# Kernel optimization log

Measured on AMD Instinct MI355X. Metric: run time of the kernel, lower is better.

Reference implementation:

```python
import jax, jax.numpy as jnp
import numpy as np

LN2 = 0.6931471805599453

def ssp(x):
    # 'shifted_sp' activation: softplus(x) - log(2)
    return jax.nn.softplus(x) - LN2

def _res_chain(x, W1, b1, W2, b2):
    # PhysNetResidual chain: x <- lin2(ssp(lin1(ssp(x)))) + x
    # W1/W2: [n_res, F, F], b1/b2: [n_res, F]
    for j in range(W1.shape[0]):
        h = ssp(x) @ W1[j] + b1[j]
        x = ssp(h) @ W2[j] + b2[j] + x
    return x

def _physnet_module(feat, radial_aev, idx12, p):
    (W_I, b_I, W_J, b_J, W_gate, gvec, W_int, b_int,
     ri_W1, ri_b1, ri_W2, ri_b2,
     ra_W1, ra_b1, ra_W2, ra_b2,
     ro_W1, ro_b1, ro_W2, ro_b2, W_out, b_out) = p
    N, F = feat.shape
    # self term (no species are dummy -> non_dummy indexing is identity)
    h_self = ssp(ssp(feat) @ W_I + b_I)                       # [N,F]
    # pair messages
    gate = radial_aev @ W_gate                                 # [P,F] (no bias)
    f12 = feat[idx12]                                          # [2,P,F] gather
    fm = ssp(ssp(f12) @ W_J + b_J)                             # [2,P,F]
    pair_msg = gate[None] * fm                                 # [2,P,F]
    proto = jnp.zeros_like(feat).at[idx12.reshape(-1)].add(
        pair_msg.reshape(-1, F))                               # scatter-add
    proto = proto + h_self
    msg = _res_chain(proto, ri_W1, ri_b1, ri_W2, ri_b2)
    feat2 = feat * gvec + ssp(msg) @ W_int + b_int
    feat2 = _res_chain(feat2, ra_W1, ra_b1, ra_W2, ra_b2)
    e = ssp(_res_chain(feat2, ro_W1, ro_b1, ro_W2, ro_b2)) @ W_out + b_out  # [N]
    return e, feat2

def setup_inputs() -> dict:
    key = jax.random.key(0)
    L, F, R = 5, 128, 64
    M, A = 128, 64
    N = M * A
    P = 400000
    ks = jax.random.split(key, 20)
    s = 0.05  # small weight scale keeps activations stable across 5 modules
    inp = {
        'species': jax.random.randint(ks[0], (M, A), 0, 4, dtype=jnp.int32),
        'features': jax.random.normal(ks[1], (N, F), jnp.float32),
        'radial_aev': jax.random.uniform(ks[2], (P, R), jnp.float32),
        'atom_index12': jax.random.randint(ks[3], (2, P), 0, N, dtype=jnp.int32),
        'W_I': jax.random.normal(ks[4], (L, F, F)) * s,
        'b_I': jnp.zeros((L, F)),
        'W_J': jax.random.normal(ks[5], (L, F, F)) * s,
        'b_J': jnp.zeros((L, F)),
        'W_gate': jax.random.normal(ks[6], (L, R, F)) * s,
        'gvec': jnp.ones((L, F)),
        'W_int': jax.random.normal(ks[7], (L, F, F)) * s,
        'b_int': jnp.zeros((L, F)),
        'ri_W1': jax.random.normal(ks[8], (L, 3, F, F)) * s,
        'ri_b1': jnp.zeros((L, 3, F)),
        'ri_W2': jax.random.normal(ks[9], (L, 3, F, F)) * s,
        'ri_b2': jnp.zeros((L, 3, F)),
        'ra_W1': jax.random.normal(ks[10], (L, 2, F, F)) * s,
        'ra_b1': jnp.zeros((L, 2, F)),
        'ra_W2': jax.random.normal(ks[11], (L, 2, F, F)) * s,
        'ra_b2': jnp.zeros((L, 2, F)),
        'ro_W1': jax.random.normal(ks[12], (L, 1, F, F)) * s,
        'ro_b1': jnp.zeros((L, 1, F)),
        'ro_W2': jax.random.normal(ks[13], (L, 1, F, F)) * s,
        'ro_b2': jnp.zeros((L, 1, F)),
        'W_out': jax.random.normal(ks[14], (L, F)) * s,
        'b_out': jnp.zeros((L,)),
    }
    return inp

def reference(species, features, radial_aev, atom_index12,
              W_I, b_I, W_J, b_J, W_gate, gvec, W_int, b_int,
              ri_W1, ri_b1, ri_W2, ri_b2,
              ra_W1, ra_b1, ra_W2, ra_b2,
              ro_W1, ro_b1, ro_W2, ro_b2, W_out, b_out):
    M, A = species.shape
    params = (W_I, b_I, W_J, b_J, W_gate, gvec, W_int, b_int,
              ri_W1, ri_b1, ri_W2, ri_b2,
              ra_W1, ra_b1, ra_W2, ra_b2,
              ro_W1, ro_b1, ro_W2, ro_b2, W_out, b_out)
    feat = features
    energies = jnp.zeros((M * A,), features.dtype)
    for l in range(W_I.shape[0]):  # fixed small module loop
        p = tuple(arr[l] for arr in params)
        e, feat = _physnet_module(feat, radial_aev, atom_index12, p)
        energies = energies + e
    return energies.reshape(M, A), feat
```

## Files before the change

### kernel.cpp

```cpp
#include <hip/hip_runtime.h>


#define LN2F 0.69314718055994530942f
#define NB 128

using short8  = __attribute__((ext_vector_type(8))) short;
using float4v = __attribute__((ext_vector_type(4))) float;
typedef const __attribute__((address_space(1))) unsigned int* gas1_t;
typedef __attribute__((address_space(3))) unsigned int* las3_t;

__device__ __forceinline__ float sspf(float x) {
  float ax = fabsf(x);
  return fmaxf(x, 0.0f) + __logf(1.0f + __expf(-ax)) - LN2F;
}

__device__ __forceinline__ unsigned short f2bf(float x) {
  return (unsigned short)((__float_as_uint(x) + 0x8000u) >> 16);
}

__device__ __forceinline__ unsigned short f2bf_ne(float x) {
  unsigned int u = __float_as_uint(x);
  u += 0x7fffu + ((u >> 16) & 1u);
  return (unsigned short)(u >> 16);
}

__device__ __forceinline__ void dma16(const void* g, void* l) {
  __builtin_amdgcn_global_load_lds((gas1_t)(unsigned long long)g,
                                   (las3_t)(unsigned long long)l, 16, 0, 0);
}

__device__ __forceinline__ void dma32k(const unsigned short* g, unsigned short* l,
                                       int w, int lane) {
  const char* gb = (const char*)g + w * 2048 + lane * 16;
  char* lb = (char*)l + w * 2048;
  dma16(gb, lb);
  dma16(gb + 1024, lb + 1024);
}
__device__ __forceinline__ void dma16k(const unsigned short* g, unsigned short* l,
                                       int w, int lane) {
  dma16((const char*)g + w * 1024 + lane * 16, (char*)l + w * 1024);
}

struct K1Args {
  const float* wsrc[80];
  int isgate[80];
  const float* bp[17];
  int bstride[17];
  const float* b_out;
  const int* idx;
  unsigned short* Wt;
  float* bias_pack;
  unsigned int* H;
  int n2p, C;
};

__global__ __launch_bounds__(256) void k1_prep(K1Args K) {
  __shared__ unsigned int h[8192];
  int b = blockIdx.x, tid = threadIdx.x;
  if (b < 80) {
    const float* s = K.wsrc[b];
    unsigned short* d = K.Wt + (size_t)b * 16384;
    if (!K.isgate[b]) {
      for (int it = 0; it < 8; ++it) {
        int q = tid + it * 256;
        int n = q & 127, j = q >> 7;
        unsigned short tmp[8];
#pragma unroll
        for (int cc = 0; cc < 8; ++cc) tmp[cc] = f2bf_ne(s[(8 * j + cc) * 128 + n]);
        *(uint4*)(d + (n * 16 + (j ^ (n & 15))) * 8) = *(uint4*)tmp;
      }
    } else {
      for (int it = 0; it < 4; ++it) {
        int q = tid + it * 256;
        int n = q & 127, j = q >> 7;
        unsigned short tmp[8];
#pragma unroll
        for (int cc = 0; cc < 8; ++cc) tmp[cc] = f2bf_ne(s[(8 * j + cc) * 128 + n]);
        *(uint4*)(d + (n * 8 + (j ^ (n & 7))) * 8) = *(uint4*)tmp;
      }
    }
  } else if (b < 85) {
    int l = b - 80;
    for (int i = tid; i < 17 * 128; i += 256) {
      int s = i >> 7;
      K.bias_pack[(size_t)l * 2304 + i] = K.bp[s][l * K.bstride[s] + (i & 127)];
    }
    if (tid == 0) K.bias_pack[(size_t)l * 2304 + 17 * 128] = K.b_out[l];
  } else {
    int blk = b - 85;
    for (int i = tid; i < 8192; i += 256) h[i] = 0;
    __syncthreads();
    int s = blk * K.C, e = min(s + K.C, K.n2p);
    for (int i = s + tid; i < e; i += 256) atomicAdd(&h[K.idx[i]], 1u);
    __syncthreads();
    for (int i = tid; i < 8192; i += 256) K.H[(size_t)blk * 8192 + i] = h[i];
  }
}

__global__ __launch_bounds__(256) void col_scan(unsigned int* __restrict__ H,
                                                unsigned int* __restrict__ tot) {
  int a = blockIdx.x * 256 + threadIdx.x;
  unsigned int run = 0;
  for (int b = 0; b < NB; ++b) {
    unsigned int v = H[(size_t)b * 8192 + a];
    H[(size_t)b * 8192 + a] = run;
    run += v;
  }
  tot[a] = run;
}

__global__ __launch_bounds__(256) void place_pass(const int* __restrict__ idx,
                                                  const unsigned int* __restrict__ H,
                                                  const unsigned int* __restrict__ tot,
                                                  unsigned int* __restrict__ off_out,
                                                  unsigned int* __restrict__ pairid,
                                                  int P, int C) {
  __shared__ unsigned int pos[8192];
  __shared__ unsigned int wt4[4];
  int b = blockIdx.x, tid = threadIdx.x;
  unsigned int local[32], s = 0;
#pragma unroll
  for (int i = 0; i < 32; ++i) { local[i] = tot[tid * 32 + i]; s += local[i]; }
  unsigned int v = s;
  int lane = tid & 63, wv = tid >> 6;
#pragma unroll
  for (int o = 1; o < 64; o <<= 1) {
    unsigned int u = __shfl_up(v, o, 64);
    if (lane >= o) v += u;
  }
  if (lane == 63) wt4[wv] = v;
  __syncthreads();
  unsigned int base = 0;
  for (int k = 0; k < wv; ++k) base += wt4[k];
  unsigned int excl = base + v - s;
#pragma unroll
  for (int i = 0; i < 32; ++i) {
    pos[tid * 32 + i] = excl;
    if (b == 0) off_out[tid * 32 + i] = excl;
    excl += local[i];
  }
  if (b == 0 && tid == 255) off_out[8192] = excl;
  __syncthreads();
  for (int i = tid; i < 8192; i += 256) pos[i] += H[(size_t)b * 8192 + i];
  __syncthreads();
  int n2p = 2 * P;
  int s2 = b * C, e2 = min(s2 + C, n2p);
  for (int i = s2 + tid; i < e2; i += 256) {
    int a = idx[i];
    unsigned int p = atomicAdd(&pos[a], 1u);
    pairid[p] = (i >= P) ? (unsigned int)(i - P) : (unsigned int)i;
  }
}

__global__ __launch_bounds__(256) void gather_kernel(const float* __restrict__ radial,
                                                     const unsigned int* __restrict__ off,
                                                     const unsigned int* __restrict__ pairid,
                                                     float* __restrict__ S) {
  __shared__ float4v red[3][16];
  int a = blockIdx.x;
  int lane = threadIdx.x & 63, w = threadIdx.x >> 6;
  int grp = lane >> 4, l16v = lane & 15;
  unsigned int b = off[a], e = off[a + 1];
  float4v acc = {0.f, 0.f, 0.f, 0.f};
  for (unsigned int base = b; base < e; base += 128) {
    unsigned int pp[8];
#pragma unroll
    for (int k = 0; k < 8; ++k) {
      unsigned int j = base + k * 16 + w * 4 + grp;
      pp[k] = pairid[j < e ? j : b];
    }
    float4v vv[8];
#pragma unroll
    for (int k = 0; k < 8; ++k)
      vv[k] = *(const float4v*)(radial + (size_t)pp[k] * 64 + l16v * 4);
#pragma unroll
    for (int k = 0; k < 8; ++k) {
      unsigned int j = base + k * 16 + w * 4 + grp;
      if (j < e) acc += vv[k];
    }
  }
#pragma unroll
  for (int o = 16; o < 64; o <<= 1) {
#pragma unroll
    for (int cc = 0; cc < 4; ++cc) acc[cc] += __shfl_xor(acc[cc], o, 64);
  }
  if (w > 0 && grp == 0) red[w - 1][l16v] = acc;
  __syncthreads();
  if (w == 0 && grp == 0) {
    acc += red[0][l16v];
    acc += red[1][l16v];
    acc += red[2][l16v];
    *(float4v*)(S + (size_t)a * 64 + l16v * 4) = acc;
  }
}

struct ChainArgs {
  const float* feat_in;
  const float* S;
  const unsigned short* wt;
  const float* bias_pack;
  float* feat_out;
  float* energy;
};

#define MFMA_ __builtin_amdgcn_mfma_f32_16x16x32_bf16

#define G128(AP, SP, ACC) { \
  short8 a0_ = *(const short8*)(aB + (AP)*4352); \
  short8 a1_ = *(const short8*)(aB + (AP)*4352 + 32); \
  short8 a2_ = *(const short8*)(aB + (AP)*4352 + 64); \
  short8 a3_ = *(const short8*)(aB + (AP)*4352 + 96); \
  ACC = MFMA_(a0_, *(const short8*)(b0 + (SP)*16384), ACC, 0, 0, 0); \
  ACC = MFMA_(a1_, *(const short8*)(b1 + (SP)*16384), ACC, 0, 0, 0); \
  ACC = MFMA_(a2_, *(const short8*)(b2 + (SP)*16384), ACC, 0, 0, 0); \
  ACC = MFMA_(a3_, *(const short8*)(b3 + (SP)*16384), ACC, 0, 0, 0); }

#define WSSPM(AP, V) { \
  wB[(AP)*4352]       = f2bf(sspf((V)[0])); \
  wB[(AP)*4352 + 136] = f2bf(sspf((V)[1])); \
  wB[(AP)*4352 + 272] = f2bf(sspf((V)[2])); \
  wB[(AP)*4352 + 408] = f2bf(sspf((V)[3])); }

#define MODBODY(S0) { \
  const float* bl = &sB[(S0)][0]; \
   \
  dma32k(wtp + 2*16384, swb[(S0)^1], w, lane); \
  gG = Z; \
  { short8 s0_ = *(const short8*)(aS); short8 s1_ = *(const short8*)(aS + 32); \
    gG = MFMA_(s0_, *(const short8*)(g0), gG, 0, 0, 0); \
    gG = MFMA_(s1_, *(const short8*)(g1), gG, 0, 0, 0); } \
  fm = Z; G128(0, (S0), fm); \
  { float bv = bl[col0]; \
    for (int r = 0; r < 4; ++r) fm[r] = sspf(fm[r] + bv); } \
  __syncthreads(); \
   \
  dma32k(wtp + 3*16384, swb[(S0)], w, lane); \
  if (l < 4) dma16k(wtp + 16*16384, sG, w, lane); \
  t4 = Z; G128(0, (S0)^1, t4); \
  { float bv = bl[128 + col0]; \
    for (int r = 0; r < 4; ++r) xf[r] = fm[r]*gG[r] + sspf(t4[r] + bv); } \
  WSSPM(1, xf); \
  __syncthreads(); \
   \
  dma32k(wtp + 4*16384, swb[(S0)^1], w, lane); \
  t4 = Z; G128(1, (S0), t4); \
  { float bv = bl[2*128 + col0]; for (int r = 0; r < 4; ++r) t4[r] += bv; } \
  WSSPM(0, t4); __syncthreads(); \
  dma32k(wtp + 5*16384, swb[(S0)], w, lane); \
  t4 = Z; G128(0, (S0)^1, t4); \
  { float bv = bl[3*128 + col0]; for (int r = 0; r < 4; ++r) xf[r] += t4[r] + bv; } \
  WSSPM(1, xf); __syncthreads(); \
  dma32k(wtp + 6*16384, swb[(S0)^1], w, lane); \
  t4 = Z; G128(1, (S0), t4); \
  { float bv = bl[4*128 + col0]; for (int r = 0; r < 4; ++r) t4[r] += bv; } \
  WSSPM(0, t4); __syncthreads(); \
  dma32k(wtp + 7*16384, swb[(S0)], w, lane); \
  t4 = Z; G128(0, (S0)^1, t4); \
  { float bv = bl[5*128 + col0]; for (int r = 0; r < 4; ++r) xf[r] += t4[r] + bv; } \
  WSSPM(1, xf); __syncthreads(); \
  dma32k(wtp + 8*16384, swb[(S0)^1], w, lane); \
  t4 = Z; G128(1, (S0), t4); \
  { float bv = bl[6*128 + col0]; for (int r = 0; r < 4; ++r) t4[r] += bv; } \
  WSSPM(0, t4); __syncthreads(); \
  dma32k(wtp + 9*16384, swb[(S0)], w, lane); \
  t4 = Z; G128(0, (S0)^1, t4); \
  { float bv = bl[7*128 + col0]; for (int r = 0; r < 4; ++r) xf[r] += t4[r] + bv; } \
  WSSPM(1, xf); __syncthreads(); \
   \
  dma32k(wtp + 10*16384, swb[(S0)^1], w, lane); \
  t4 = Z; G128(1, (S0), t4); \
  { float bv = bl[8*128 + col0]; float gv = bl[15*128 + col0]; \
    for (int r = 0; r < 4; ++r) xf[r] = ff[r]*gv + t4[r] + bv; } \
  WSSPM(0, xf); __syncthreads(); \
   \
  dma32k(wtp + 11*16384, swb[(S0)], w, lane); \
  t4 = Z; G128(0, (S0)^1, t4); \
  { float bv = bl[9*128 + col0]; for (int r = 0; r < 4; ++r) t4[r] += bv; } \
  WSSPM(1, t4); __syncthreads(); \
  dma32k(wtp + 12*16384, swb[(S0)^1], w, lane); \
  t4 = Z; G128(1, (S0), t4); \
  { float bv = bl[10*128 + col0]; for (int r = 0; r < 4; ++r) xf[r] += t4[r] + bv; } \
  WSSPM(0, xf); __syncthreads(); \
  dma32k(wtp + 13*16384, swb[(S0)], w, lane); \
  t4 = Z; G128(0, (S0)^1, t4); \
  { float bv = bl[11*128 + col0]; for (int r = 0; r < 4; ++r) t4[r] += bv; } \
  WSSPM(1, t4); __syncthreads(); \
  dma32k(wtp + 14*16384, swb[(S0)^1], w, lane); \
  if (l < 4 && w < 9) \
    dma16((const char*)A.bias_pack + (size_t)(l + 1) * 9216 + w * 1024 + lane * 16, \
          (char*)&sB[(S0)^1][0] + w * 1024); \
  t4 = Z; G128(1, (S0), t4); \
  { float bv = bl[12*128 + col0]; for (int r = 0; r < 4; ++r) xf[r] += t4[r] + bv; } \
  WSSPM(0, xf); __syncthreads(); \
  ff = xf; \
  if (l == 4) { \
    for (int r = 0; r < 4; ++r) \
      A.feat_out[(size_t)(row0 + arow + quad*4 + r) * 128 + col0] = xf[r]; \
  } \
   \
  dma32k(wtp + 15*16384, swb[(S0)], w, lane); \
  t4 = Z; G128(0, (S0)^1, t4); \
  { float bv = bl[13*128 + col0]; for (int r = 0; r < 4; ++r) t4[r] += bv; } \
  WSSPM(1, t4); __syncthreads(); \
   \
  if (l < 4) dma32k(wtp + 17*16384, swb[(S0)^1], w, lane); \
  t4 = Z; G128(1, (S0), t4); \
  { float bv = bl[14*128 + col0]; float wv = bl[16*128 + col0]; \
    p0 += sspf(xf[0] + t4[0] + bv) * wv; \
    p1 += sspf(xf[1] + t4[1] + bv) * wv; \
    p2 += sspf(xf[2] + t4[2] + bv) * wv; \
    p3 += sspf(xf[3] + t4[3] + bv) * wv; } \
  bsum += bl[17*128]; \
  __syncthreads(); }

__global__ __launch_bounds__(1024, 4) void chain_kernel(ChainArgs A) {
  __shared__ __align__(16) unsigned short swb[2][16384];
  __shared__ __align__(16) unsigned short sG[8192];
  __shared__ __align__(16) unsigned short sA[2][32 * 136];
  __shared__ __align__(16) unsigned short sS[32 * 72];
  __shared__ __align__(16) float sB[2][2304];
  __shared__ float sE[32];

  const int tid  = threadIdx.x;
  const int row0 = blockIdx.x * 32;
  const int lane = tid & 63;
  const int w    = tid >> 6;
  const int g    = w >> 3;
  const int c    = w & 7;
  const int l16  = lane & 15;
  const int quad = lane >> 4;
  const int arow = 16 * g;
  const int col0 = 16 * c + l16;
  const int l8   = l16 & 7;

  const unsigned short* aB = &sA[0][0] + (arow + l16) * 136 + quad * 8;
  unsigned short*       wB = &sA[0][0] + (arow + quad * 4) * 136 + col0;
  const unsigned short* b0 = &swb[0][0] + col0 * 128 + (((quad + 0) ^ l16) * 8);
  const unsigned short* b1 = &swb[0][0] + col0 * 128 + (((quad + 4) ^ l16) * 8);
  const unsigned short* b2 = &swb[0][0] + col0 * 128 + (((quad + 8) ^ l16) * 8);
  const unsigned short* b3 = &swb[0][0] + col0 * 128 + (((quad + 12) ^ l16) * 8);
  const unsigned short* aS = &sS[0] + (arow + l16) * 72 + quad * 8;
  const unsigned short* g0 = &sG[0] + col0 * 64 + (((quad + 0) ^ l8) * 8);
  const unsigned short* g1 = &sG[0] + col0 * 64 + (((quad + 4) ^ l8) * 8);

  dma16k(A.wt, sG, w, lane);
  dma32k(A.wt + 16384, swb[0], w, lane);
  if (w < 9)
    dma16((const char*)A.bias_pack + w * 1024 + lane * 16, (char*)&sB[0][0] + w * 1024);

  for (int i = tid; i < 32 * 64; i += 1024) {
    int r = i >> 6, k = i & 63;
    sS[r * 72 + k] = f2bf(A.S[(size_t)(row0 + r) * 64 + k]);
  }
  for (int i = tid; i < 32 * 128; i += 1024) {
    int r = i >> 7, k = i & 127;
    sA[0][r * 136 + k] = f2bf(sspf(A.feat_in[(size_t)(row0 + r) * 128 + k]));
  }
  float4v ff;
#pragma unroll
  for (int r = 0; r < 4; ++r)
    ff[r] = A.feat_in[(size_t)(row0 + arow + quad * 4 + r) * 128 + col0];
  if (tid < 32) sE[tid] = 0.0f;
  __syncthreads();

  const float4v Z = {0.f, 0.f, 0.f, 0.f};
  float4v gG, fm, xf, t4;
  float p0 = 0.f, p1 = 0.f, p2 = 0.f, p3 = 0.f, bsum = 0.f;

#pragma unroll 1
  for (int l = 0; l < 5; ++l) {
    const unsigned short* wtp = A.wt + (size_t)l * 16 * 16384;
    if ((l & 1) == 0) MODBODY(0) else MODBODY(1)
  }

#pragma unroll
  for (int o = 1; o < 16; o <<= 1) {
    p0 += __shfl_xor(p0, o, 64);
    p1 += __shfl_xor(p1, o, 64);
    p2 += __shfl_xor(p2, o, 64);
    p3 += __shfl_xor(p3, o, 64);
  }
  if (l16 == 0) {
    atomicAdd(&sE[arow + quad * 4 + 0], p0);
    atomicAdd(&sE[arow + quad * 4 + 1], p1);
    atomicAdd(&sE[arow + quad * 4 + 2], p2);
    atomicAdd(&sE[arow + quad * 4 + 3], p3);
  }
  __syncthreads();
  if (tid < 32) A.energy[row0 + tid] = sE[tid] + bsum;
}

extern "C" void kernel_launch(void* const* d_in, const int* in_sizes, int n_in,
                              void* d_out, int out_size, void* d_ws, size_t ws_size,
                              hipStream_t stream) {
  const float* features = (const float*)d_in[1];
  const float* radial   = (const float*)d_in[2];
  const int*   idx12    = (const int*)  d_in[3];
  const float* W_I    = (const float*)d_in[4];
  const float* b_I    = (const float*)d_in[5];
  const float* W_J    = (const float*)d_in[6];
  const float* b_J    = (const float*)d_in[7];
  const float* W_gate = (const float*)d_in[8];
  const float* gvec   = (const float*)d_in[9];
  const float* W_int  = (const float*)d_in[10];
  const float* b_int  = (const float*)d_in[11];
  const float* ri_W1  = (const float*)d_in[12];
  const float* ri_b1  = (const float*)d_in[13];
  const float* ri_W2  = (const float*)d_in[14];
  const float* ri_b2  = (const float*)d_in[15];
  const float* ra_W1  = (const float*)d_in[16];
  const float* ra_b1  = (const float*)d_in[17];
  const float* ra_W2  = (const float*)d_in[18];
  const float* ra_b2  = (const float*)d_in[19];
  const float* ro_W1  = (const float*)d_in[20];
  const float* ro_b1  = (const float*)d_in[21];
  const float* ro_W2  = (const float*)d_in[22];
  const float* ro_b2  = (const float*)d_in[23];
  const float* W_out  = (const float*)d_in[24];
  const float* b_out  = (const float*)d_in[25];

  const int N = in_sizes[1] / 128;
  const int P = in_sizes[3] / 2;
  const int L = in_sizes[25];
  const int n2p = 2 * P;
  const int C = (n2p + NB - 1) / NB;

  float* S = (float*)d_ws;
  float* bias_pack = S + (size_t)N * 64;
  unsigned short* Wt = (unsigned short*)(bias_pack + 5 * 2304);
  unsigned int* H      = (unsigned int*)(Wt + (size_t)80 * 16384);
  unsigned int* tot    = H + (size_t)NB * 8192;
  unsigned int* off    = tot + N;
  unsigned int* pairid = off + N + 4;

  K1Args k1;
  for (int l = 0; l < L; ++l) {
    const float* fx[16] = {
      W_gate + l * 8192,
      W_J + l * 16384, W_I + l * 16384,
      ri_W1 + (l * 3 + 0) * 16384, ri_W2 + (l * 3 + 0) * 16384,
      ri_W1 + (l * 3 + 1) * 16384, ri_W2 + (l * 3 + 1) * 16384,
      ri_W1 + (l * 3 + 2) * 16384, ri_W2 + (l * 3 + 2) * 16384,
      W_int + l * 16384,
      ra_W1 + (l * 2 + 0) * 16384, ra_W2 + (l * 2 + 0) * 16384,
      ra_W1 + (l * 2 + 1) * 16384, ra_W2 + (l * 2 + 1) * 16384,
      ro_W1 + l * 16384, ro_W2 + l * 16384 };
    for (int t = 0; t < 16; ++t) { k1.wsrc[l * 16 + t] = fx[t]; k1.isgate[l * 16 + t] = (t == 0); }
  }
  const float* bp[17] = { b_J, b_I,
    ri_b1, ri_b2, ri_b1 + 128, ri_b2 + 128, ri_b1 + 256, ri_b2 + 256,
    b_int, ra_b1, ra_b2, ra_b1 + 128, ra_b2 + 128, ro_b1, ro_b2, gvec, W_out };
  int st[17] = {128,128, 384,384,384,384,384,384, 128, 256,256,256,256, 128,128,128,128};
  for (int q = 0; q < 17; ++q) { k1.bp[q] = bp[q]; k1.bstride[q] = st[q]; }
  k1.b_out = b_out;
  k1.idx = idx12; k1.Wt = Wt; k1.bias_pack = bias_pack; k1.H = H;
  k1.n2p = n2p; k1.C = C;
  k1_prep<<<80 + 5 + NB, 256, 0, stream>>>(k1);

  col_scan<<<32, 256, 0, stream>>>(H, tot);
  place_pass<<<NB, 256, 0, stream>>>(idx12, H, tot, off, pairid, P, C);
  gather_kernel<<<N, 256, 0, stream>>>(radial, off, pairid, S);

  ChainArgs ca;
  ca.feat_in   = features;
  ca.S         = S;
  ca.wt        = Wt;
  ca.bias_pack = bias_pack;
  ca.energy    = (float*)d_out;
  ca.feat_out  = (float*)d_out + N;
  chain_kernel<<<N / 32, 1024, 0, stream>>>(ca);
}
```

Baseline: 328.8 us.

## Fuse preprocessing kernels into one cooperative kernel with grid syncs

Merges weight conversion, bias packing, histogram, column scan, placement and radial gather into a single cooperative kernel of 256 blocks of 1024 threads, separated by grid-wide syncs. It also parallelises the column scan across 32 row segments per column instead of one thread walking all 128 rows. The aim is to remove launch gaps and the serial scan. The trade-off is that grid.sync barriers are added, and the gather now runs on only 256 blocks rather than one block per atom, which may reduce memory-level parallelism.

```diff
diff --git a/kernel.cpp b/kernel.cpp
--- a/kernel.cpp
+++ b/kernel.cpp
@@ -1,4 +1,7 @@
 #include <hip/hip_runtime.h>
+#include <hip/hip_cooperative_groups.h>
+
+namespace cg = cooperative_groups;
 
 
 #define LN2F 0.69314718055994530942f
@@ -41,28 +44,44 @@
   dma16((const char*)g + w * 1024 + lane * 16, (char*)l + w * 1024);
 }
 
-struct K1Args {
+struct SArgs {
   const float* wsrc[80];
   int isgate[80];
   const float* bp[17];
   int bstride[17];
   const float* b_out;
   const int* idx;
+  const float* radial;
   unsigned short* Wt;
   float* bias_pack;
   unsigned int* H;
-  int n2p, C;
+  unsigned int* tot;
+  unsigned int* off;
+  unsigned int* pairid;
+  float* S;
+  int P, n2p, C;
 };
 
-__global__ __launch_bounds__(256) void k1_prep(K1Args K) {
-  __shared__ unsigned int h[8192];
-  int b = blockIdx.x, tid = threadIdx.x;
-  if (b < 80) {
-    const float* s = K.wsrc[b];
-    unsigned short* d = K.Wt + (size_t)b * 16384;
-    if (!K.isgate[b]) {
-      for (int it = 0; it < 8; ++it) {
-        int q = tid + it * 256;
+__global__ __launch_bounds__(1024) void s_all(SArgs K) {
+  __shared__ unsigned int shst[8192];
+  __shared__ unsigned int wtt[16];
+  cg::grid_group grid = cg::this_grid();
+  const int b = blockIdx.x, tid = threadIdx.x;
+
+  if (b < NB) {
+    for (int i = tid; i < 8192; i += 1024) shst[i] = 0;
+    __syncthreads();
+    int s = b * K.C, e = min(s + K.C, K.n2p);
+    for (int i = s + tid; i < e; i += 1024) atomicAdd(&shst[K.idx[i]], 1u);
+    __syncthreads();
+    for (int i = tid; i < 8192; i += 1024) K.H[(size_t)b * 8192 + i] = shst[i];
+  } else if (b < NB + 80) {
+    int m = b - NB;
+    const float* s = K.wsrc[m];
+    unsigned short* d = K.Wt + (size_t)m * 16384;
+    if (!K.isgate[m]) {
+      for (int it = 0; it < 2; ++it) {
+        int q = tid + it * 1024;
         int n = q & 127, j = q >> 7;
         unsigned short tmp[8];
 #pragma unroll
@@ -70,127 +89,123 @@
         *(uint4*)(d + (n * 16 + (j ^ (n & 15))) * 8) = *(uint4*)tmp;
       }
     } else {
-      for (int it = 0; it < 4; ++it) {
-        int q = tid + it * 256;
-        int n = q & 127, j = q >> 7;
-        unsigned short tmp[8];
-#pragma unroll
-        for (int cc = 0; cc < 8; ++cc) tmp[cc] = f2bf_ne(s[(8 * j + cc) * 128 + n]);
-        *(uint4*)(d + (n * 8 + (j ^ (n & 7))) * 8) = *(uint4*)tmp;
-      }
-    }
-  } else if (b < 85) {
-    int l = b - 80;
-    for (int i = tid; i < 17 * 128; i += 256) {
+      int n = tid & 127, j = tid >> 7;
+      unsigned short tmp[8];
+#pragma unroll
+      for (int cc = 0; cc < 8; ++cc) tmp[cc] = f2bf_ne(s[(8 * j + cc) * 128 + n]);
+      *(uint4*)(d + (n * 8 + (j ^ (n & 7))) * 8) = *(uint4*)tmp;
+    }
+  } else if (b < NB + 85) {
+    int l = b - (NB + 80);
+    for (int i = tid; i < 17 * 128; i += 1024) {
       int s = i >> 7;
       K.bias_pack[(size_t)l * 2304 + i] = K.bp[s][l * K.bstride[s] + (i & 127)];
     }
     if (tid == 0) K.bias_pack[(size_t)l * 2304 + 17 * 128] = K.b_out[l];
-  } else {
-    int blk = b - 85;
-    for (int i = tid; i < 8192; i += 256) h[i] = 0;
-    __syncthreads();
-    int s = blk * K.C, e = min(s + K.C, K.n2p);
-    for (int i = s + tid; i < e; i += 256) atomicAdd(&h[K.idx[i]], 1u);
-    __syncthreads();
-    for (int i = tid; i < 8192; i += 256) K.H[(size_t)blk * 8192 + i] = h[i];
-  }
-}
-
-__global__ __launch_bounds__(256) void col_scan(unsigned int* __restrict__ H,
-                                                unsigned int* __restrict__ tot) {
-  int a = blockIdx.x * 256 + threadIdx.x;
-  unsigned int run = 0;
-  for (int b = 0; b < NB; ++b) {
-    unsigned int v = H[(size_t)b * 8192 + a];
-    H[(size_t)b * 8192 + a] = run;
-    run += v;
-  }
-  tot[a] = run;
-}
-
-__global__ __launch_bounds__(256) void place_pass(const int* __restrict__ idx,
-                                                  const unsigned int* __restrict__ H,
-                                                  const unsigned int* __restrict__ tot,
-                                                  unsigned int* __restrict__ off_out,
-                                                  unsigned int* __restrict__ pairid,
-                                                  int P, int C) {
-  __shared__ unsigned int pos[8192];
-  __shared__ unsigned int wt4[4];
-  int b = blockIdx.x, tid = threadIdx.x;
-  unsigned int local[32], s = 0;
-#pragma unroll
-  for (int i = 0; i < 32; ++i) { local[i] = tot[tid * 32 + i]; s += local[i]; }
-  unsigned int v = s;
-  int lane = tid & 63, wv = tid >> 6;
-#pragma unroll
-  for (int o = 1; o < 64; o <<= 1) {
-    unsigned int u = __shfl_up(v, o, 64);
-    if (lane >= o) v += u;
-  }
-  if (lane == 63) wt4[wv] = v;
-  __syncthreads();
-  unsigned int base = 0;
-  for (int k = 0; k < wv; ++k) base += wt4[k];
-  unsigned int excl = base + v - s;
-#pragma unroll
-  for (int i = 0; i < 32; ++i) {
-    pos[tid * 32 + i] = excl;
-    if (b == 0) off_out[tid * 32 + i] = excl;
-    excl += local[i];
-  }
-  if (b == 0 && tid == 255) off_out[8192] = excl;
-  __syncthreads();
-  for (int i = tid; i < 8192; i += 256) pos[i] += H[(size_t)b * 8192 + i];
-  __syncthreads();
-  int n2p = 2 * P;
-  int s2 = b * C, e2 = min(s2 + C, n2p);
-  for (int i = s2 + tid; i < e2; i += 256) {
-    int a = idx[i];
-    unsigned int p = atomicAdd(&pos[a], 1u);
-    pairid[p] = (i >= P) ? (unsigned int)(i - P) : (unsigned int)i;
-  }
-}
-
-__global__ __launch_bounds__(256) void gather_kernel(const float* __restrict__ radial,
-                                                     const unsigned int* __restrict__ off,
-                                                     const unsigned int* __restrict__ pairid,
-                                                     float* __restrict__ S) {
-  __shared__ float4v red[3][16];
-  int a = blockIdx.x;
-  int lane = threadIdx.x & 63, w = threadIdx.x >> 6;
-  int grp = lane >> 4, l16v = lane & 15;
-  unsigned int b = off[a], e = off[a + 1];
-  float4v acc = {0.f, 0.f, 0.f, 0.f};
-  for (unsigned int base = b; base < e; base += 128) {
-    unsigned int pp[8];
-#pragma unroll
-    for (int k = 0; k < 8; ++k) {
-      unsigned int j = base + k * 16 + w * 4 + grp;
-      pp[k] = pairid[j < e ? j : b];
-    }
-    float4v vv[8];
-#pragma unroll
-    for (int k = 0; k < 8; ++k)
-      vv[k] = *(const float4v*)(radial + (size_t)pp[k] * 64 + l16v * 4);
-#pragma unroll
-    for (int k = 0; k < 8; ++k) {
-      unsigned int j = base + k * 16 + w * 4 + grp;
-      if (j < e) acc += vv[k];
-    }
-  }
-#pragma unroll
-  for (int o = 16; o < 64; o <<= 1) {
-#pragma unroll
-    for (int cc = 0; cc < 4; ++cc) acc[cc] += __shfl_xor(acc[cc], o, 64);
-  }
-  if (w > 0 && grp == 0) red[w - 1][l16v] = acc;
-  __syncthreads();
-  if (w == 0 && grp == 0) {
-    acc += red[0][l16v];
-    acc += red[1][l16v];
-    acc += red[2][l16v];
-    *(float4v*)(S + (size_t)a * 64 + l16v * 4) = acc;
+  }
+  __threadfence();
+  grid.sync();
+
+  {
+    unsigned int (*part)[33] = (unsigned int(*)[33])shst;
+    const int c = tid & 31, sgm = tid >> 5;
+    const int col = b * 32 + c;
+    unsigned int psum = 0;
+#pragma unroll
+    for (int r = sgm * 4; r < sgm * 4 + 4; ++r)
+      psum += K.H[(size_t)r * 8192 + col];
+    part[sgm][c] = psum;
+    __syncthreads();
+    if (tid < 32) {
+      unsigned int run = 0;
+#pragma unroll
+      for (int s2 = 0; s2 < 32; ++s2) {
+        unsigned int v = part[s2][tid];
+        part[s2][tid] = run;
+        run += v;
+      }
+      K.tot[b * 32 + tid] = run;
+    }
+    __syncthreads();
+    unsigned int run = part[sgm][c];
+#pragma unroll
+    for (int r = sgm * 4; r < sgm * 4 + 4; ++r) {
+      unsigned int v = K.H[(size_t)r * 8192 + col];
+      K.H[(size_t)r * 8192 + col] = run;
+      run += v;
+    }
+  }
+  __threadfence();
+  grid.sync();
+
+  if (b < NB) {
+    unsigned int loc[8], ssum = 0;
+#pragma unroll
+    for (int i = 0; i < 8; ++i) { loc[i] = K.tot[tid * 8 + i]; ssum += loc[i]; }
+    unsigned int v = ssum;
+    const int lane = tid & 63, wv2 = tid >> 6;
+#pragma unroll
+    for (int o = 1; o < 64; o <<= 1) {
+      unsigned int u = __shfl_up(v, o, 64);
+      if (lane >= o) v += u;
+    }
+    if (lane == 63) wtt[wv2] = v;
+    __syncthreads();
+    unsigned int base2 = 0;
+    for (int k = 0; k < wv2; ++k) base2 += wtt[k];
+    unsigned int excl = base2 + v - ssum;
+#pragma unroll
+    for (int i = 0; i < 8; ++i) {
+      unsigned int a = tid * 8 + i;
+      if (b == 0) K.off[a] = excl;
+      shst[a] = excl + K.H[(size_t)b * 8192 + a];
+      excl += loc[i];
+    }
+    if (b == 0 && tid == 1023) K.off[8192] = excl;
+    __syncthreads();
+    int s3 = b * K.C, e3 = min(s3 + K.C, K.n2p);
+    for (int i = s3 + tid; i < e3; i += 1024) {
+      int a = K.idx[i];
+      unsigned int p = atomicAdd(&shst[a], 1u);
+      K.pairid[p] = (i >= K.P) ? (unsigned int)(i - K.P) : (unsigned int)i;
+    }
+  }
+  __threadfence();
+  grid.sync();
+
+  {
+    const int wv = tid >> 6, lane = tid & 63;
+    const int grp = lane >> 4, l16v = lane & 15;
+#pragma unroll 1
+    for (int j2 = 0; j2 < 2; ++j2) {
+      int a = b * 32 + wv * 2 + j2;
+      unsigned int bb = K.off[a], ee = K.off[a + 1];
+      float4v acc = {0.f, 0.f, 0.f, 0.f};
+      for (unsigned int base = bb; base < ee; base += 32) {
+        unsigned int pp[8];
+#pragma unroll
+        for (int k = 0; k < 8; ++k) {
+          unsigned int j = base + k * 4 + grp;
+          pp[k] = K.pairid[j < ee ? j : bb];
+        }
+        float4v vv[8];
+#pragma unroll
+        for (int k = 0; k < 8; ++k)
+          vv[k] = *(const float4v*)(K.radial + (size_t)pp[k] * 64 + l16v * 4);
+#pragma unroll
+        for (int k = 0; k < 8; ++k) {
+          unsigned int j = base + k * 4 + grp;
+          if (j < ee) acc += vv[k];
+        }
+      }
+#pragma unroll
+      for (int o = 16; o < 64; o <<= 1) {
+#pragma unroll
+        for (int cc = 0; cc < 4; ++cc) acc[cc] += __shfl_xor(acc[cc], o, 64);
+      }
+      if (grp == 0)
+        *(float4v*)(K.S + (size_t)a * 64 + l16v * 4) = acc;
+    }
   }
 }
 
@@ -433,7 +448,7 @@
   unsigned int* off    = tot + N;
   unsigned int* pairid = off + N + 4;
 
-  K1Args k1;
+  SArgs sa;
   for (int l = 0; l < L; ++l) {
     const float* fx[16] = {
       W_gate + l * 8192,
@@ -445,21 +460,22 @@
       ra_W1 + (l * 2 + 0) * 16384, ra_W2 + (l * 2 + 0) * 16384,
       ra_W1 + (l * 2 + 1) * 16384, ra_W2 + (l * 2 + 1) * 16384,
       ro_W1 + l * 16384, ro_W2 + l * 16384 };
-    for (int t = 0; t < 16; ++t) { k1.wsrc[l * 16 + t] = fx[t]; k1.isgate[l * 16 + t] = (t == 0); }
+    for (int t = 0; t < 16; ++t) { sa.wsrc[l * 16 + t] = fx[t]; sa.isgate[l * 16 + t] = (t == 0); }
   }
   const float* bp[17] = { b_J, b_I,
     ri_b1, ri_b2, ri_b1 + 128, ri_b2 + 128, ri_b1 + 256, ri_b2 + 256,
     b_int, ra_b1, ra_b2, ra_b1 + 128, ra_b2 + 128, ro_b1, ro_b2, gvec, W_out };
   int st[17] = {128,128, 384,384,384,384,384,384, 128, 256,256,256,256, 128,128,128,128};
-  for (int q = 0; q < 17; ++q) { k1.bp[q] = bp[q]; k1.bstride[q] = st[q]; }
-  k1.b_out = b_out;
-  k1.idx = idx12; k1.Wt = Wt; k1.bias_pack = bias_pack; k1.H = H;
-  k1.n2p = n2p; k1.C = C;
-  k1_prep<<<80 + 5 + NB, 256, 0, stream>>>(k1);
-
-  col_scan<<<32, 256, 0, stream>>>(H, tot);
-  place_pass<<<NB, 256, 0, stream>>>(idx12, H, tot, off, pairid, P, C);
-  gather_kernel<<<N, 256, 0, stream>>>(radial, off, pairid, S);
+  for (int q = 0; q < 17; ++q) { sa.bp[q] = bp[q]; sa.bstride[q] = st[q]; }
+  sa.b_out = b_out;
+  sa.idx = idx12; sa.radial = radial;
+  sa.Wt = Wt; sa.bias_pack = bias_pack;
+  sa.H = H; sa.tot = tot; sa.off = off; sa.pairid = pairid; sa.S = S;
+  sa.P = P; sa.n2p = n2p; sa.C = C;
+
+  void* kargs[] = { (void*)&sa };
+  hipLaunchCooperativeKernel((const void*)s_all, dim3(256), dim3(1024),
+                             kargs, 0, stream);
 
   ChainArgs ca;
   ca.feat_in   = features;
```

After: 748.2 us. +127.5%, slower.

## Load MFMA weight fragments straight from global into registers instead of LDS staging

Applied to the files above, without the earlier changes.

The prep kernel now writes weights in a per-lane MFMA fragment order, so each wave in the chain kernel can load its B operands directly from global or L2 into registers, double-buffered across layers. The LDS weight, gate and bias buffers and the async global-to-LDS copies are removed. Barriers become raw s_barrier calls guarded by sched barriers and an explicit lgkmcnt wait, so they no longer wait on outstanding global loads. The intent is to cut LDS traffic and LDS footprint and to let weight loads overlap across barriers. The cost is more VGPRs and a global or L2 latency on each weight fragment load, since every block now fetches the weights repeatedly from cache.

```diff
diff --git a/kernel.cpp b/kernel.cpp
--- a/kernel.cpp
+++ b/kernel.cpp
@@ -6,8 +6,6 @@
 
 using short8  = __attribute__((ext_vector_type(8))) short;
 using float4v = __attribute__((ext_vector_type(4))) float;
-typedef const __attribute__((address_space(1))) unsigned int* gas1_t;
-typedef __attribute__((address_space(3))) unsigned int* las3_t;
 
 __device__ __forceinline__ float sspf(float x) {
   float ax = fabsf(x);
@@ -22,23 +20,6 @@
   unsigned int u = __float_as_uint(x);
   u += 0x7fffu + ((u >> 16) & 1u);
   return (unsigned short)(u >> 16);
-}
-
-__device__ __forceinline__ void dma16(const void* g, void* l) {
-  __builtin_amdgcn_global_load_lds((gas1_t)(unsigned long long)g,
-                                   (las3_t)(unsigned long long)l, 16, 0, 0);
-}
-
-__device__ __forceinline__ void dma32k(const unsigned short* g, unsigned short* l,
-                                       int w, int lane) {
-  const char* gb = (const char*)g + w * 2048 + lane * 16;
-  char* lb = (char*)l + w * 2048;
-  dma16(gb, lb);
-  dma16(gb + 1024, lb + 1024);
-}
-__device__ __forceinline__ void dma16k(const unsigned short* g, unsigned short* l,
-                                       int w, int lane) {
-  dma16((const char*)g + w * 1024 + lane * 16, (char*)l + w * 1024);
 }
 
 struct K1Args {
@@ -62,21 +43,25 @@
     unsigned short* d = K.Wt + (size_t)b * 16384;
     if (!K.isgate[b]) {
       for (int it = 0; it < 8; ++it) {
-        int q = tid + it * 256;
-        int n = q & 127, j = q >> 7;
+        int id = tid + it * 256;
+        int lane = id & 63, mm = (id >> 6) & 3, c8 = id >> 8;
+        int l16 = lane & 15, quad = lane >> 4;
+        int n = 16 * c8 + l16, k0 = 8 * (4 * mm + quad);
         unsigned short tmp[8];
 #pragma unroll
-        for (int cc = 0; cc < 8; ++cc) tmp[cc] = f2bf_ne(s[(8 * j + cc) * 128 + n]);
-        *(uint4*)(d + (n * 16 + (j ^ (n & 15))) * 8) = *(uint4*)tmp;
+        for (int cc = 0; cc < 8; ++cc) tmp[cc] = f2bf_ne(s[(k0 + cc) * 128 + n]);
+        *(uint4*)(d + c8 * 2048 + mm * 512 + lane * 8) = *(uint4*)tmp;
       }
     } else {
       for (int it = 0; it < 4; ++it) {
-        int q = tid + it * 256;
-        int n = q & 127, j = q >> 7;
+        int id = tid + it * 256;
+        int lane = id & 63, mm = (id >> 6) & 1, c8 = id >> 7;
+        int l16 = lane & 15, quad = lane >> 4;
+        int n = 16 * c8 + l16, k0 = 8 * (4 * mm + quad);
         unsigned short tmp[8];
 #pragma unroll
-        for (int cc = 0; cc < 8; ++cc) tmp[cc] = f2bf_ne(s[(8 * j + cc) * 128 + n]);
-        *(uint4*)(d + (n * 8 + (j ^ (n & 7))) * 8) = *(uint4*)tmp;
+        for (int cc = 0; cc < 8; ++cc) tmp[cc] = f2bf_ne(s[(k0 + cc) * 128 + n]);
+        *(uint4*)(d + c8 * 1024 + mm * 512 + lane * 8) = *(uint4*)tmp;
       }
     }
   } else if (b < 85) {
@@ -205,15 +190,27 @@
 
 #define MFMA_ __builtin_amdgcn_mfma_f32_16x16x32_bf16
 
-#define G128(AP, SP, ACC) { \
+#define BAR() { __builtin_amdgcn_sched_barrier(0); \
+  asm volatile("s_waitcnt lgkmcnt(0)" ::: "memory"); \
+  __builtin_amdgcn_s_barrier(); \
+  __builtin_amdgcn_sched_barrier(0); }
+
+#define LDW(WP, sp) { \
+  const unsigned short* wp_ = (sp) + woff; \
+  W[WP][0] = *(const short8*)(wp_); \
+  W[WP][1] = *(const short8*)(wp_ + 512); \
+  W[WP][2] = *(const short8*)(wp_ + 1024); \
+  W[WP][3] = *(const short8*)(wp_ + 1536); }
+
+#define G128R(AP, WP, ACC) { \
   short8 a0_ = *(const short8*)(aB + (AP)*4352); \
   short8 a1_ = *(const short8*)(aB + (AP)*4352 + 32); \
   short8 a2_ = *(const short8*)(aB + (AP)*4352 + 64); \
   short8 a3_ = *(const short8*)(aB + (AP)*4352 + 96); \
-  ACC = MFMA_(a0_, *(const short8*)(b0 + (SP)*16384), ACC, 0, 0, 0); \
-  ACC = MFMA_(a1_, *(const short8*)(b1 + (SP)*16384), ACC, 0, 0, 0); \
-  ACC = MFMA_(a2_, *(const short8*)(b2 + (SP)*16384), ACC, 0, 0, 0); \
-  ACC = MFMA_(a3_, *(const short8*)(b3 + (SP)*16384), ACC, 0, 0, 0); }
+  ACC = MFMA_(a0_, W[WP][0], ACC, 0, 0, 0); \
+  ACC = MFMA_(a1_, W[WP][1], ACC, 0, 0, 0); \
+  ACC = MFMA_(a2_, W[WP][2], ACC, 0, 0, 0); \
+  ACC = MFMA_(a3_, W[WP][3], ACC, 0, 0, 0); }
 
 #define WSSPM(AP, V) { \
   wB[(AP)*4352]       = f2bf(sspf((V)[0])); \
@@ -222,103 +219,98 @@
   wB[(AP)*4352 + 408] = f2bf(sspf((V)[3])); }
 
 #define MODBODY(S0) { \
-  const float* bl = &sB[(S0)][0]; \
-   \
-  dma32k(wtp + 2*16384, swb[(S0)^1], w, lane); \
-  gG = Z; \
-  { short8 s0_ = *(const short8*)(aS); short8 s1_ = *(const short8*)(aS + 32); \
-    gG = MFMA_(s0_, *(const short8*)(g0), gG, 0, 0, 0); \
-    gG = MFMA_(s1_, *(const short8*)(g1), gG, 0, 0, 0); } \
-  fm = Z; G128(0, (S0), fm); \
-  { float bv = bl[col0]; \
-    for (int r = 0; r < 4; ++r) fm[r] = sspf(fm[r] + bv); } \
-  __syncthreads(); \
-   \
-  dma32k(wtp + 3*16384, swb[(S0)], w, lane); \
-  if (l < 4) dma16k(wtp + 16*16384, sG, w, lane); \
-  t4 = Z; G128(0, (S0)^1, t4); \
-  { float bv = bl[128 + col0]; \
-    for (int r = 0; r < 4; ++r) xf[r] = fm[r]*gG[r] + sspf(t4[r] + bv); } \
-  WSSPM(1, xf); \
-  __syncthreads(); \
-   \
-  dma32k(wtp + 4*16384, swb[(S0)^1], w, lane); \
-  t4 = Z; G128(1, (S0), t4); \
-  { float bv = bl[2*128 + col0]; for (int r = 0; r < 4; ++r) t4[r] += bv; } \
-  WSSPM(0, t4); __syncthreads(); \
-  dma32k(wtp + 5*16384, swb[(S0)], w, lane); \
-  t4 = Z; G128(0, (S0)^1, t4); \
-  { float bv = bl[3*128 + col0]; for (int r = 0; r < 4; ++r) xf[r] += t4[r] + bv; } \
-  WSSPM(1, xf); __syncthreads(); \
-  dma32k(wtp + 6*16384, swb[(S0)^1], w, lane); \
-  t4 = Z; G128(1, (S0), t4); \
-  { float bv = bl[4*128 + col0]; for (int r = 0; r < 4; ++r) t4[r] += bv; } \
-  WSSPM(0, t4); __syncthreads(); \
-  dma32k(wtp + 7*16384, swb[(S0)], w, lane); \
-  t4 = Z; G128(0, (S0)^1, t4); \
-  { float bv = bl[5*128 + col0]; for (int r = 0; r < 4; ++r) xf[r] += t4[r] + bv; } \
-  WSSPM(1, xf); __syncthreads(); \
-  dma32k(wtp + 8*16384, swb[(S0)^1], w, lane); \
-  t4 = Z; G128(1, (S0), t4); \
-  { float bv = bl[6*128 + col0]; for (int r = 0; r < 4; ++r) t4[r] += bv; } \
-  WSSPM(0, t4); __syncthreads(); \
-  dma32k(wtp + 9*16384, swb[(S0)], w, lane); \
-  t4 = Z; G128(0, (S0)^1, t4); \
-  { float bv = bl[7*128 + col0]; for (int r = 0; r < 4; ++r) xf[r] += t4[r] + bv; } \
-  WSSPM(1, xf); __syncthreads(); \
-   \
-  dma32k(wtp + 10*16384, swb[(S0)^1], w, lane); \
-  t4 = Z; G128(1, (S0), t4); \
-  { float bv = bl[8*128 + col0]; float gv = bl[15*128 + col0]; \
-    for (int r = 0; r < 4; ++r) xf[r] = ff[r]*gv + t4[r] + bv; } \
-  WSSPM(0, xf); __syncthreads(); \
-   \
-  dma32k(wtp + 11*16384, swb[(S0)], w, lane); \
-  t4 = Z; G128(0, (S0)^1, t4); \
-  { float bv = bl[9*128 + col0]; for (int r = 0; r < 4; ++r) t4[r] += bv; } \
-  WSSPM(1, t4); __syncthreads(); \
-  dma32k(wtp + 12*16384, swb[(S0)^1], w, lane); \
-  t4 = Z; G128(1, (S0), t4); \
-  { float bv = bl[10*128 + col0]; for (int r = 0; r < 4; ++r) xf[r] += t4[r] + bv; } \
-  WSSPM(0, xf); __syncthreads(); \
-  dma32k(wtp + 13*16384, swb[(S0)], w, lane); \
-  t4 = Z; G128(0, (S0)^1, t4); \
-  { float bv = bl[11*128 + col0]; for (int r = 0; r < 4; ++r) t4[r] += bv; } \
-  WSSPM(1, t4); __syncthreads(); \
-  dma32k(wtp + 14*16384, swb[(S0)^1], w, lane); \
-  if (l < 4 && w < 9) \
-    dma16((const char*)A.bias_pack + (size_t)(l + 1) * 9216 + w * 1024 + lane * 16, \
-          (char*)&sB[(S0)^1][0] + w * 1024); \
-  t4 = Z; G128(1, (S0), t4); \
-  { float bv = bl[12*128 + col0]; for (int r = 0; r < 4; ++r) xf[r] += t4[r] + bv; } \
-  WSSPM(0, xf); __syncthreads(); \
+  const float* bp = A.bias_pack + l * 2304; \
+   \
+  { float bv_ = bp[col0]; \
+    LDW((S0)^1, wtp + 2*16384); \
+    gG = Z; \
+    { short8 s0_ = *(const short8*)(aS); short8 s1_ = *(const short8*)(aS + 32); \
+      gG = MFMA_(s0_, GT0, gG, 0, 0, 0); \
+      gG = MFMA_(s1_, GT1, gG, 0, 0, 0); } \
+    fm = Z; G128R(0, (S0), fm); \
+    for (int r = 0; r < 4; ++r) fm[r] = sspf(fm[r] + bv_); } \
+   \
+  { float bv_ = bp[128 + col0]; \
+    LDW((S0), wtp + 3*16384); \
+    if (l < 4) { \
+      GT0 = *(const short8*)(wtp + 16*16384 + goff); \
+      GT1 = *(const short8*)(wtp + 16*16384 + goff + 512); \
+    } \
+    t4 = Z; G128R(0, (S0)^1, t4); \
+    for (int r = 0; r < 4; ++r) xf[r] = fm[r] * gG[r] + sspf(t4[r] + bv_); } \
+  WSSPM(1, xf); BAR(); \
+   \
+  { float bv_ = bp[2*128 + col0]; LDW((S0)^1, wtp + 4*16384); \
+    t4 = Z; G128R(1, (S0), t4); \
+    for (int r = 0; r < 4; ++r) t4[r] += bv_; } \
+  WSSPM(0, t4); BAR(); \
+  { float bv_ = bp[3*128 + col0]; LDW((S0), wtp + 5*16384); \
+    t4 = Z; G128R(0, (S0)^1, t4); \
+    for (int r = 0; r < 4; ++r) xf[r] += t4[r] + bv_; } \
+  WSSPM(1, xf); BAR(); \
+  { float bv_ = bp[4*128 + col0]; LDW((S0)^1, wtp + 6*16384); \
+    t4 = Z; G128R(1, (S0), t4); \
+    for (int r = 0; r < 4; ++r) t4[r] += bv_; } \
+  WSSPM(0, t4); BAR(); \
+  { float bv_ = bp[5*128 + col0]; LDW((S0), wtp + 7*16384); \
+    t4 = Z; G128R(0, (S0)^1, t4); \
+    for (int r = 0; r < 4; ++r) xf[r] += t4[r] + bv_; } \
+  WSSPM(1, xf); BAR(); \
+  { float bv_ = bp[6*128 + col0]; LDW((S0)^1, wtp + 8*16384); \
+    t4 = Z; G128R(1, (S0), t4); \
+    for (int r = 0; r < 4; ++r) t4[r] += bv_; } \
+  WSSPM(0, t4); BAR(); \
+  { float bv_ = bp[7*128 + col0]; LDW((S0), wtp + 9*16384); \
+    t4 = Z; G128R(0, (S0)^1, t4); \
+    for (int r = 0; r < 4; ++r) xf[r] += t4[r] + bv_; } \
+  WSSPM(1, xf); BAR(); \
+   \
+  { float bv_ = bp[8*128 + col0]; float gv_ = bp[15*128 + col0]; \
+    LDW((S0)^1, wtp + 10*16384); \
+    t4 = Z; G128R(1, (S0), t4); \
+    for (int r = 0; r < 4; ++r) xf[r] = ff[r] * gv_ + t4[r] + bv_; } \
+  WSSPM(0, xf); BAR(); \
+   \
+  { float bv_ = bp[9*128 + col0]; LDW((S0), wtp + 11*16384); \
+    t4 = Z; G128R(0, (S0)^1, t4); \
+    for (int r = 0; r < 4; ++r) t4[r] += bv_; } \
+  WSSPM(1, t4); BAR(); \
+  { float bv_ = bp[10*128 + col0]; LDW((S0)^1, wtp + 12*16384); \
+    t4 = Z; G128R(1, (S0), t4); \
+    for (int r = 0; r < 4; ++r) xf[r] += t4[r] + bv_; } \
+  WSSPM(0, xf); BAR(); \
+  { float bv_ = bp[11*128 + col0]; LDW((S0), wtp + 13*16384); \
+    t4 = Z; G128R(0, (S0)^1, t4); \
+    for (int r = 0; r < 4; ++r) t4[r] += bv_; } \
+  WSSPM(1, t4); BAR(); \
+  { float bv_ = bp[12*128 + col0]; LDW((S0)^1, wtp + 14*16384); \
+    t4 = Z; G128R(1, (S0), t4); \
+    for (int r = 0; r < 4; ++r) xf[r] += t4[r] + bv_; } \
+  WSSPM(0, xf); BAR(); \
   ff = xf; \
   if (l == 4) { \
     for (int r = 0; r < 4; ++r) \
       A.feat_out[(size_t)(row0 + arow + quad*4 + r) * 128 + col0] = xf[r]; \
   } \
    \
-  dma32k(wtp + 15*16384, swb[(S0)], w, lane); \
-  t4 = Z; G128(0, (S0)^1, t4); \
-  { float bv = bl[13*128 + col0]; for (int r = 0; r < 4; ++r) t4[r] += bv; } \
-  WSSPM(1, t4); __syncthreads(); \
-   \
-  if (l < 4) dma32k(wtp + 17*16384, swb[(S0)^1], w, lane); \
-  t4 = Z; G128(1, (S0), t4); \
-  { float bv = bl[14*128 + col0]; float wv = bl[16*128 + col0]; \
-    p0 += sspf(xf[0] + t4[0] + bv) * wv; \
-    p1 += sspf(xf[1] + t4[1] + bv) * wv; \
-    p2 += sspf(xf[2] + t4[2] + bv) * wv; \
-    p3 += sspf(xf[3] + t4[3] + bv) * wv; } \
-  bsum += bl[17*128]; \
-  __syncthreads(); }
+  { float bv_ = bp[13*128 + col0]; LDW((S0), wtp + 15*16384); \
+    t4 = Z; G128R(0, (S0)^1, t4); \
+    for (int r = 0; r < 4; ++r) t4[r] += bv_; } \
+  WSSPM(1, t4); BAR(); \
+   \
+  { float bv_ = bp[14*128 + col0]; float wv_ = bp[16*128 + col0]; \
+    if (l < 4) LDW((S0)^1, wtp + 17*16384); \
+    t4 = Z; G128R(1, (S0), t4); \
+    p0 += sspf(xf[0] + t4[0] + bv_) * wv_; \
+    p1 += sspf(xf[1] + t4[1] + bv_) * wv_; \
+    p2 += sspf(xf[2] + t4[2] + bv_) * wv_; \
+    p3 += sspf(xf[3] + t4[3] + bv_) * wv_; } \
+  bsum += bp[17*128]; \
+  BAR(); }
 
 __global__ __launch_bounds__(1024, 4) void chain_kernel(ChainArgs A) {
-  __shared__ __align__(16) unsigned short swb[2][16384];
-  __shared__ __align__(16) unsigned short sG[8192];
   __shared__ __align__(16) unsigned short sA[2][32 * 136];
   __shared__ __align__(16) unsigned short sS[32 * 72];
-  __shared__ __align__(16) float sB[2][2304];
   __shared__ float sE[32];
 
   const int tid  = threadIdx.x;
@@ -331,22 +323,19 @@
   const int quad = lane >> 4;
   const int arow = 16 * g;
   const int col0 = 16 * c + l16;
-  const int l8   = l16 & 7;
+
+  const int woff = c * 2048 + lane * 8;
+  const int goff = c * 1024 + lane * 8;
 
   const unsigned short* aB = &sA[0][0] + (arow + l16) * 136 + quad * 8;
   unsigned short*       wB = &sA[0][0] + (arow + quad * 4) * 136 + col0;
-  const unsigned short* b0 = &swb[0][0] + col0 * 128 + (((quad + 0) ^ l16) * 8);
-  const unsigned short* b1 = &swb[0][0] + col0 * 128 + (((quad + 4) ^ l16) * 8);
-  const unsigned short* b2 = &swb[0][0] + col0 * 128 + (((quad + 8) ^ l16) * 8);
-  const unsigned short* b3 = &swb[0][0] + col0 * 128 + (((quad + 12) ^ l16) * 8);
   const unsigned short* aS = &sS[0] + (arow + l16) * 72 + quad * 8;
-  const unsigned short* g0 = &sG[0] + col0 * 64 + (((quad + 0) ^ l8) * 8);
-  const unsigned short* g1 = &sG[0] + col0 * 64 + (((quad + 4) ^ l8) * 8);
-
-  dma16k(A.wt, sG, w, lane);
-  dma32k(A.wt + 16384, swb[0], w, lane);
-  if (w < 9)
-    dma16((const char*)A.bias_pack + w * 1024 + lane * 16, (char*)&sB[0][0] + w * 1024);
+
+  short8 GT0, GT1;
+  short8 W[2][4];
+  GT0 = *(const short8*)(A.wt + goff);
+  GT1 = *(const short8*)(A.wt + goff + 512);
+  LDW(0, A.wt + 16384);
 
   for (int i = tid; i < 32 * 64; i += 1024) {
     int r = i >> 6, k = i & 63;
@@ -386,7 +375,7 @@
     atomicAdd(&sE[arow + quad * 4 + 2], p2);
     atomicAdd(&sE[arow + quad * 4 + 3], p3);
   }
-  __syncthreads();
+  BAR();
   if (tid < 32) A.energy[row0 + tid] = sE[tid] + bsum;
 }
 
```

Measured after the change: 351.6 us. 6.9% more time.
